# Performance work log

Hardware: AMD Instinct MI355X
Metric: run time of the kernel (lower is better)

Reference implementation:

```python
import jax, jax.numpy as jnp
import numpy as np

GAMMA = 1.0  # init arg gamma


def setup_inputs() -> dict:
    key = jax.random.key(0)
    k1, k2 = jax.random.split(key, 2)
    B, D, U = 8192, 512, 4096
    x = jax.random.normal(k1, (B, D), dtype=jnp.float32)
    kernel = jax.random.normal(k2, (D, U), dtype=jnp.float32) * 0.05  # glorot-ish scale
    bias = jnp.zeros((U,), dtype=jnp.float32)
    return {"x": x, "kernel": kernel, "bias": bias}


def reference(x, kernel, bias):
    # Original: distance = ||x[b,:] - kernel[:,u]||_2 over input_dim, out = exp(-gamma*distance^2) + bias.
    # Use the algebraic cdist expansion ||a-b||^2 = |a|^2 + |b|^2 - 2 a.b to avoid
    # materializing the (B, D, U) broadcast tensor the TF code creates.
    x_sq = jnp.sum(x * x, axis=-1, keepdims=True)          # (B, 1)
    k_sq = jnp.sum(kernel * kernel, axis=0)[None, :]       # (1, U)
    d2 = x_sq + k_sq - 2.0 * (x @ kernel)                  # (B, U) squared distances
    d2 = jnp.maximum(d2, 0.0)                              # guard tiny negatives from cancellation
    return jnp.exp(-GAMMA * d2) + bias                     # activation is None (linear)
```

## Files before the change

### kernel.cpp

```cpp
#include <hip/hip_runtime.h>
#include <hip/hip_bf16.h>
#include <stdint.h>


using short8 = __attribute__((ext_vector_type(8))) short;
using bf16x8 = __attribute__((ext_vector_type(8))) __bf16;
using f32x4  = __attribute__((ext_vector_type(4))) float;
typedef unsigned short ushort_t;

#define GAMMA_F 1.0f

__device__ __forceinline__ ushort_t f2bf(float f) {
  unsigned u = __float_as_uint(f);
  u = (u + 0x7fffu + ((u >> 16) & 1u)) >> 16;
  return (ushort_t)u;
}

__global__ __launch_bounds__(256) void prep_kernel(
    const float* __restrict__ x, const float* __restrict__ kern,
    ushort_t* __restrict__ xb, ushort_t* __restrict__ kbT,
    float* __restrict__ xsq, float* __restrict__ ksq) {
  const int t = threadIdx.x;
  if (blockIdx.x < 2048) {
    const int w = t >> 6, l = t & 63;
    const int r = blockIdx.x * 4 + w;
    const float4* xr = (const float4*)(x + (size_t)r * 512);
    float4 v0 = xr[l * 2 + 0];
    float4 v1 = xr[l * 2 + 1];
    float s = v0.x * v0.x + v0.y * v0.y + v0.z * v0.z + v0.w * v0.w
            + v1.x * v1.x + v1.y * v1.y + v1.z * v1.z + v1.w * v1.w;
    short8 p;
    p[0] = (short)f2bf(v0.x); p[1] = (short)f2bf(v0.y);
    p[2] = (short)f2bf(v0.z); p[3] = (short)f2bf(v0.w);
    p[4] = (short)f2bf(v1.x); p[5] = (short)f2bf(v1.y);
    p[6] = (short)f2bf(v1.z); p[7] = (short)f2bf(v1.w);
    *(short8*)(xb + (size_t)r * 512 + l * 8) = p;
#pragma unroll
    for (int o = 32; o > 0; o >>= 1) s += __shfl_xor(s, o);
    if (l == 0) xsq[r] = s;
  } else {
    __shared__ ushort_t tile[64][65];
    __shared__ float red[4][64];
    const int u0 = (blockIdx.x - 2048) * 64;
    const int c = t & 63, tq = t >> 6;
    float part = 0.f;
    for (int d0 = 0; d0 < 512; d0 += 64) {
#pragma unroll
      for (int i = 0; i < 16; ++i) {
        const int r = tq * 16 + i;
        const float v = kern[(size_t)(d0 + r) * 4096 + u0 + c];
        part += v * v;
        tile[r][c] = f2bf(v);
      }
      __syncthreads();
      const int dl = (t & 7) * 8;
#pragma unroll
      for (int h = 0; h < 2; ++h) {
        const int ul = (t >> 3) + h * 32;
        short8 v;
#pragma unroll
        for (int j = 0; j < 8; ++j) ((ushort_t*)&v)[j] = tile[dl + j][ul];
        *(short8*)(kbT + (size_t)(u0 + ul) * 512 + d0 + dl) = v;
      }
      __syncthreads();
    }
    red[tq][c] = part;
    __syncthreads();
    if (t < 64) ksq[u0 + t] = red[0][t] + red[1][t] + red[2][t] + red[3][t];
  }
}

__global__ __launch_bounds__(256, 2) void rbf_gemm_kernel(
    const ushort_t* __restrict__ xb, const ushort_t* __restrict__ kbT,
    const float* __restrict__ xsq, const float* __restrict__ ksq,
    const float* __restrict__ bias, float* __restrict__ out) {
  __shared__ ushort_t A_lds[2 * 128 * 64];
  __shared__ ushort_t B_lds[2 * 128 * 64];

  const int tid = threadIdx.x;
  const int w = tid >> 6, l = tid & 63;
  const int wr = w >> 1, wc = w & 1;

  const int wgid = ((blockIdx.x & 7) << 8) + (blockIdx.x >> 3);
  const int brow = (wgid >> 5) * 128;
  const int bcol = (wgid & 31) * 128;

  const int srow = tid >> 3;
  const int sj = (tid & 7) ^ ((tid >> 3) & 7);
  const ushort_t* gA0 = xb  + (size_t)(brow + srow) * 512 + sj * 8;
  const ushort_t* gB0 = kbT + (size_t)(bcol + srow) * 512 + sj * 8;
  const int ldsw = w * 512;

#define STAGE_TILE(kt, dn) do {                                                   \
    const ushort_t* _ga = gA0 + (size_t)(kt) * 64;                                \
    const ushort_t* _gb = gB0 + (size_t)(kt) * 64;                                \
    const int _lb = (dn) * 8192 + ldsw;                                           \
    _Pragma("unroll")                                                             \
    for (int i = 0; i < 4; ++i)                                                   \
      __builtin_amdgcn_global_load_lds(                                           \
          (const __attribute__((address_space(1))) void*)(_ga + (size_t)i * 16384),\
          (__attribute__((address_space(3))) void*)(&A_lds[_lb + i * 2048]), 16, 0, 0); \
    _Pragma("unroll")                                                             \
    for (int i = 0; i < 4; ++i)                                                   \
      __builtin_amdgcn_global_load_lds(                                           \
          (const __attribute__((address_space(1))) void*)(_gb + (size_t)i * 16384),\
          (__attribute__((address_space(3))) void*)(&B_lds[_lb + i * 2048]), 16, 0, 0); \
  } while (0)

  const int l15 = l & 15, l4 = l >> 4, l7 = l & 7;
  const int chk0 = (l4 ^ l7) * 8;
  const int chk1 = ((4 + l4) ^ l7) * 8;
  const int aoff = (wr * 64 + l15) * 64;
  const int boff = (wc * 64 + l15) * 64;

  f32x4 acc[4][4] = {};

  STAGE_TILE(0, 0);

#pragma unroll 2
  for (int s = 0; s < 8; ++s) {
    const int dbase = (s & 1) * 8192;
    STAGE_TILE((s + 1) & 7, (s + 1) & 1);
    asm volatile("s_waitcnt vmcnt(8)" ::: "memory");
    asm volatile("s_barrier" ::: "memory");

    bf16x8 a0[4], a1[4], b0[4], b1[4];
#pragma unroll
    for (int m = 0; m < 4; ++m) {
      a0[m] = *(const bf16x8*)&A_lds[dbase + aoff + m * 1024 + chk0];
      a1[m] = *(const bf16x8*)&A_lds[dbase + aoff + m * 1024 + chk1];
    }
#pragma unroll
    for (int n = 0; n < 4; ++n) {
      b0[n] = *(const bf16x8*)&B_lds[dbase + boff + n * 1024 + chk0];
      b1[n] = *(const bf16x8*)&B_lds[dbase + boff + n * 1024 + chk1];
    }
    __builtin_amdgcn_s_setprio(1);
#pragma unroll
    for (int m = 0; m < 4; ++m)
#pragma unroll
      for (int n = 0; n < 4; ++n)
        acc[m][n] = __builtin_amdgcn_mfma_f32_16x16x32_bf16(a0[m], b0[n], acc[m][n], 0, 0, 0);
#pragma unroll
    for (int m = 0; m < 4; ++m)
#pragma unroll
      for (int n = 0; n < 4; ++n)
        acc[m][n] = __builtin_amdgcn_mfma_f32_16x16x32_bf16(a1[m], b1[n], acc[m][n], 0, 0, 0);
    __builtin_amdgcn_s_setprio(0);
    __builtin_amdgcn_sched_barrier(0);
    asm volatile("s_barrier" ::: "memory");
  }

  const int cl = l15, rg = l4 * 4;
#pragma unroll
  for (int n = 0; n < 4; ++n) {
    const int gc = bcol + wc * 64 + n * 16 + cl;
    const float kq = ksq[gc];
    const float bz = bias[gc];
#pragma unroll
    for (int m = 0; m < 4; ++m) {
      const int gr0 = brow + wr * 64 + m * 16 + rg;
      const float4 xq = *(const float4*)&xsq[gr0];
      const float xq4[4] = {xq.x, xq.y, xq.z, xq.w};
#pragma unroll
      for (int j = 0; j < 4; ++j) {
        float d2 = xq4[j] + kq - 2.0f * acc[m][n][j];
        d2 = fmaxf(d2, 0.0f);
        out[(size_t)(gr0 + j) * 4096 + gc] = __expf(-GAMMA_F * d2) + bz;
      }
    }
  }
#undef STAGE_TILE
}

__global__ __launch_bounds__(256) void rbf_direct_kernel(
    const float* __restrict__ x, const float* __restrict__ kern,
    const float* __restrict__ bias, float* __restrict__ out) {
  __shared__ float Xs[64][17];
  __shared__ float Ks[16][65];
  const int tid = threadIdx.x;
  const int brow = blockIdx.y * 64, bcol = blockIdx.x * 64;
  const int tr = (tid >> 4) * 4, tc = (tid & 15) * 4;
  float acc[4][4] = {};
  for (int k0 = 0; k0 < 512; k0 += 16) {
    {
      const int r = tid >> 2, c = (tid & 3) * 4;
      float4 v = *(const float4*)&x[(size_t)(brow + r) * 512 + k0 + c];
      Xs[r][c] = v.x; Xs[r][c + 1] = v.y; Xs[r][c + 2] = v.z; Xs[r][c + 3] = v.w;
    }
    {
      const int r = tid >> 4, c = (tid & 15) * 4;
      float4 v = *(const float4*)&kern[(size_t)(k0 + r) * 4096 + bcol + c];
      Ks[r][c] = v.x; Ks[r][c + 1] = v.y; Ks[r][c + 2] = v.z; Ks[r][c + 3] = v.w;
    }
    __syncthreads();
#pragma unroll
    for (int kk = 0; kk < 16; ++kk) {
      float a[4], b[4];
#pragma unroll
      for (int i = 0; i < 4; ++i) a[i] = Xs[tr + i][kk];
#pragma unroll
      for (int j = 0; j < 4; ++j) b[j] = Ks[kk][tc + j];
#pragma unroll
      for (int i = 0; i < 4; ++i)
#pragma unroll
        for (int j = 0; j < 4; ++j) {
          float d = a[i] - b[j];
          acc[i][j] = fmaf(d, d, acc[i][j]);
        }
    }
    __syncthreads();
  }
#pragma unroll
  for (int i = 0; i < 4; ++i)
#pragma unroll
    for (int j = 0; j < 4; ++j)
      out[(size_t)(brow + tr + i) * 4096 + bcol + tc + j] =
          __expf(-GAMMA_F * acc[i][j]) + bias[bcol + tc + j];
}

extern "C" void kernel_launch(void* const* d_in, const int* in_sizes, int n_in,
                              void* d_out, int out_size, void* d_ws, size_t ws_size,
                              hipStream_t stream) {
  const float* x    = (const float*)d_in[0];
  const float* kern = (const float*)d_in[1];
  const float* bias = (const float*)d_in[2];
  float* out = (float*)d_out;

  const size_t NEED = 8388608  + 4194304  + 32768  + 16384 ;
  if (ws_size < NEED) {
    rbf_direct_kernel<<<dim3(64, 128), 256, 0, stream>>>(x, kern, bias, out);
    return;
  }

  char* ws = (char*)d_ws;
  ushort_t* xb  = (ushort_t*)(ws);
  ushort_t* kbT = (ushort_t*)(ws + 8388608);
  float* xsq = (float*)(ws + 8388608 + 4194304);
  float* ksq = xsq + 8192;

  prep_kernel<<<2112, 256, 0, stream>>>(x, kern, xb, kbT, xsq, ksq);
  rbf_gemm_kernel<<<2048, 256, 0, stream>>>(xb, kbT, xsq, ksq, bias, out);
}
```

Baseline: 200.2 us.

## Use 256x128 tiles with 8 waves and drop LDS double buffering

The GEMM workgroup grows to 512 threads computing a 256x128 output tile, so half as many blocks are launched and each loaded B tile is reused across twice as many rows. The double-buffered LDS prefetch pipeline is replaced by a single buffer with load, sync, compute, sync per k-step, cutting LDS use to allow more resident blocks. The cost is that global-to-LDS loads no longer overlap MFMA work within a block, so latency hiding now depends on other resident blocks.

```diff
diff --git a/kernel.cpp b/kernel.cpp
--- a/kernel.cpp
+++ b/kernel.cpp
@@ -70,19 +70,19 @@
   }
 }
 
-__global__ __launch_bounds__(256, 2) void rbf_gemm_kernel(
+__global__ __launch_bounds__(512, 4) void rbf_gemm_kernel(
     const ushort_t* __restrict__ xb, const ushort_t* __restrict__ kbT,
     const float* __restrict__ xsq, const float* __restrict__ ksq,
     const float* __restrict__ bias, float* __restrict__ out) {
-  __shared__ ushort_t A_lds[2 * 128 * 64];
-  __shared__ ushort_t B_lds[2 * 128 * 64];
+  __shared__ ushort_t A_lds[256 * 64];
+  __shared__ ushort_t B_lds[128 * 64];
 
   const int tid = threadIdx.x;
   const int w = tid >> 6, l = tid & 63;
   const int wr = w >> 1, wc = w & 1;
 
-  const int wgid = ((blockIdx.x & 7) << 8) + (blockIdx.x >> 3);
-  const int brow = (wgid >> 5) * 128;
+  const int wgid = ((blockIdx.x & 7) << 7) + (blockIdx.x >> 3);
+  const int brow = (wgid >> 5) * 256;
   const int bcol = (wgid & 31) * 128;
 
   const int srow = tid >> 3;
@@ -91,20 +91,19 @@
   const ushort_t* gB0 = kbT + (size_t)(bcol + srow) * 512 + sj * 8;
   const int ldsw = w * 512;
 
-#define STAGE_TILE(kt, dn) do {                                                   \
+#define STAGE_TILE(kt) do {                                                       \
     const ushort_t* _ga = gA0 + (size_t)(kt) * 64;                                \
     const ushort_t* _gb = gB0 + (size_t)(kt) * 64;                                \
-    const int _lb = (dn) * 8192 + ldsw;                                           \
     _Pragma("unroll")                                                             \
     for (int i = 0; i < 4; ++i)                                                   \
       __builtin_amdgcn_global_load_lds(                                           \
-          (const __attribute__((address_space(1))) void*)(_ga + (size_t)i * 16384),\
-          (__attribute__((address_space(3))) void*)(&A_lds[_lb + i * 2048]), 16, 0, 0); \
+          (const __attribute__((address_space(1))) void*)(_ga + (size_t)i * 32768),\
+          (__attribute__((address_space(3))) void*)(&A_lds[i * 4096 + ldsw]), 16, 0, 0); \
     _Pragma("unroll")                                                             \
-    for (int i = 0; i < 4; ++i)                                                   \
+    for (int i = 0; i < 2; ++i)                                                   \
       __builtin_amdgcn_global_load_lds(                                           \
-          (const __attribute__((address_space(1))) void*)(_gb + (size_t)i * 16384),\
-          (__attribute__((address_space(3))) void*)(&B_lds[_lb + i * 2048]), 16, 0, 0); \
+          (const __attribute__((address_space(1))) void*)(_gb + (size_t)i * 32768),\
+          (__attribute__((address_space(3))) void*)(&B_lds[i * 4096 + ldsw]), 16, 0, 0); \
   } while (0)
 
   const int l15 = l & 15, l4 = l >> 4, l7 = l & 7;
@@ -115,25 +114,20 @@
 
   f32x4 acc[4][4] = {};
 
-  STAGE_TILE(0, 0);
-
-#pragma unroll 2
   for (int s = 0; s < 8; ++s) {
-    const int dbase = (s & 1) * 8192;
-    STAGE_TILE((s + 1) & 7, (s + 1) & 1);
-    asm volatile("s_waitcnt vmcnt(8)" ::: "memory");
-    asm volatile("s_barrier" ::: "memory");
+    STAGE_TILE(s);
+    __syncthreads();
 
     bf16x8 a0[4], a1[4], b0[4], b1[4];
 #pragma unroll
     for (int m = 0; m < 4; ++m) {
-      a0[m] = *(const bf16x8*)&A_lds[dbase + aoff + m * 1024 + chk0];
-      a1[m] = *(const bf16x8*)&A_lds[dbase + aoff + m * 1024 + chk1];
+      a0[m] = *(const bf16x8*)&A_lds[aoff + m * 1024 + chk0];
+      a1[m] = *(const bf16x8*)&A_lds[aoff + m * 1024 + chk1];
     }
 #pragma unroll
     for (int n = 0; n < 4; ++n) {
-      b0[n] = *(const bf16x8*)&B_lds[dbase + boff + n * 1024 + chk0];
-      b1[n] = *(const bf16x8*)&B_lds[dbase + boff + n * 1024 + chk1];
+      b0[n] = *(const bf16x8*)&B_lds[boff + n * 1024 + chk0];
+      b1[n] = *(const bf16x8*)&B_lds[boff + n * 1024 + chk1];
     }
     __builtin_amdgcn_s_setprio(1);
 #pragma unroll
@@ -147,8 +141,7 @@
       for (int n = 0; n < 4; ++n)
         acc[m][n] = __builtin_amdgcn_mfma_f32_16x16x32_bf16(a1[m], b1[n], acc[m][n], 0, 0, 0);
     __builtin_amdgcn_s_setprio(0);
-    __builtin_amdgcn_sched_barrier(0);
-    asm volatile("s_barrier" ::: "memory");
+    __syncthreads();
   }
 
   const int cl = l15, rg = l4 * 4;
@@ -240,5 +233,5 @@
   float* ksq = xsq + 8192;
 
   prep_kernel<<<2112, 256, 0, stream>>>(x, kern, xb, kbT, xsq, ksq);
-  rbf_gemm_kernel<<<2048, 256, 0, stream>>>(xb, kbT, xsq, ksq, bias, out);
-}
+  rbf_gemm_kernel<<<1024, 512, 0, stream>>>(xb, kbT, xsq, ksq, bias, out);
+}
```

Result: slower. 254.1 us (+26.9%).
